# Performance work log

Measured on AMD Instinct MI355X. Metric: run time of the kernel, lower is better.

Reference implementation:

```python
import jax, jax.numpy as jnp
import numpy as np

N_NODES = 50000
N_EDGES = 600000
N_ELEMENTS = 100
N_RBF = 50
D = 128
CUTOFF = 5.0


def setup_inputs() -> dict:
    key = jax.random.key(0)
    ks = jax.random.split(key, 10)
    node_type = jax.random.randint(ks[0], (N_NODES,), 0, N_ELEMENTS)
    x_nodes = jax.random.normal(ks[1], (N_NODES, D), dtype=jnp.float32)
    src = jax.random.randint(ks[2], (N_EDGES,), 0, N_NODES)
    dst = jax.random.randint(ks[3], (N_EDGES,), 0, N_NODES)
    rbf_edges = jax.random.normal(ks[4], (N_EDGES, N_RBF), dtype=jnp.float32)
    dist = jax.random.uniform(ks[5], (N_EDGES,), dtype=jnp.float32) * (CUTOFF * 1.2)
    emb = jax.random.normal(ks[6], (N_ELEMENTS, D), dtype=jnp.float32) * 0.1
    W_e = jax.random.normal(ks[7], (D, N_RBF), dtype=jnp.float32) * (1.0 / np.sqrt(N_RBF))
    b_e = jnp.zeros((D,), dtype=jnp.float32)
    W_c = jax.random.normal(ks[8], (D, 2 * D), dtype=jnp.float32) * (1.0 / np.sqrt(2 * D))
    b_c = jnp.zeros((D,), dtype=jnp.float32)
    return {"node_type": node_type, "x_nodes": x_nodes, "src": src, "dst": dst,
            "rbf_edges": rbf_edges, "dist": dist, "emb": emb,
            "W_e": W_e, "b_e": b_e, "W_c": W_c, "b_c": b_c}


def cosine_cutoff(dist, cutoff):
    # 0.5*(cos(pi*d/cutoff)+1), zeroed beyond cutoff
    w = 0.5 * (jnp.cos(dist * (jnp.pi / cutoff)) + 1.0)
    return w * (dist < cutoff).astype(dist.dtype)


def reference(node_type, x_nodes, src, dst, rbf_edges, dist, emb, W_e, b_e, W_c, b_c):
    # node embedding from atom type: [N, D]
    x_neighbors = emb[node_type]
    # edge projection weighted by cutoff: [E, D]
    x_edges = (rbf_edges @ W_e.T + b_e) * cosine_cutoff(dist, CUTOFF)[:, None]
    # gather source node embedding, multiply by edge embedding, scatter-sum to dst
    msg = x_neighbors[src] * x_edges  # [E, D]
    x_integrated = jax.ops.segment_sum(msg, dst, num_segments=N_NODES)  # [N, D]
    # concat + combine linear: [N, D]
    x_combine = jnp.concatenate([x_nodes, x_integrated], axis=-1)
    return x_combine @ W_c.T + b_c
```

## Files before the change

kernel.cpp:

```cpp
#include <hip/hip_runtime.h>
#include <hip/hip_bf16.h>

constexpr int NN   = 50000;
constexpr int NE   = 600000;
constexpr int NRBF = 50;
constexpr int DIM  = 128;
constexpr float CUT = 5.0f;
constexpr float PI_F = 3.14159265358979323846f;

constexpr int CAP = 32;

constexpr size_t OFF_DEG   = 0;
constexpr size_t OFF_OVFC  = (size_t)NN * 4;
constexpr size_t OFF_EBUF  = 200960;
constexpr size_t OFF_OVF   = OFF_EBUF + (size_t)NN * CAP * 16;
constexpr size_t OFF_WAUG  = OFF_OVF  + (size_t)NE * 4;
constexpr size_t OFF_EPERM = OFF_WAUG + 128 * 64 * 2;
constexpr size_t OFF_WCB   = OFF_EPERM + 100 * 128 * 2;


typedef __attribute__((ext_vector_type(4))) float f32x4;
typedef __attribute__((ext_vector_type(8))) short short8;

__device__ __forceinline__ float bf2f(unsigned short u) {
    return __uint_as_float(((unsigned int)u) << 16);
}
__device__ __forceinline__ unsigned short f2bf(float f) {
    return __bfloat16_as_ushort(__float2bfloat16(f));
}

__global__ __launch_bounds__(256)
void bucket_prep(const int* __restrict__ dst, const float* __restrict__ dist,
                 const int* __restrict__ src, const int* __restrict__ node_type,
                 int* __restrict__ deg, int4* __restrict__ ebuf,
                 int* __restrict__ ovf, int* __restrict__ ovf_cnt,
                 const float* __restrict__ W_e, const float* __restrict__ b_e,
                 const float* __restrict__ emb, const float* __restrict__ W_c,
                 unsigned short* __restrict__ W_aug, unsigned short* __restrict__ emb_perm,
                 unsigned short* __restrict__ W_cb)
{
    const int e = blockIdx.x * 256 + threadIdx.x;

    if (e < NE) {
        const float dd = dist[e];
        if (dd < CUT) {
            const float w = 0.5f * (__cosf(dd * (PI_F / CUT)) + 1.0f);
            const int n = dst[e];
            const int pos = atomicAdd(&deg[n], 1);
            if (pos < CAP) {
                ebuf[(size_t)n * CAP + pos] =
                    make_int4(e, __float_as_int(w), node_type[src[e]], 0);
            } else {
                ovf[atomicAdd(ovf_cnt, 1)] = e;
            }
        }
    }

    if (e < 128 * 64) {
        const int d = e >> 6, k = e & 63;
        float v = 0.0f;
        if (k < NRBF)       v = W_e[d * NRBF + k];
        else if (k == NRBF) v = b_e[d];
        W_aug[e] = f2bf(v);
    } else if (e < 128 * 64 + 100 * 128) {
        const int i = e - 128 * 64;
        const int tau = i >> 7, p = i & 127;
        const int d = 16 * (p & 7) + (p >> 3);
        emb_perm[i] = f2bf(emb[tau * DIM + d]);
    } else if (e < 128 * 64 + 100 * 128 + 128 * 256) {
        const int i = e - (128 * 64 + 100 * 128);
        W_cb[i] = f2bf(W_c[i]);
    }
}

struct NodeLoad {
    float2 r0, r1, r2, r3, q0, q1, q2, q3;
    float  ccl;
    int    degn;
    int    mb;
};

__device__ __forceinline__ void issue_node(const int4* __restrict__ eb_s,
                                           const int* __restrict__ deg_s,
                                           const float* __restrict__ rbf,
                                           int nl, int c, int g, NodeLoad& L)
{
    const int dn = deg_s[nl];
    L.degn = dn < CAP ? dn : CAP;
    L.mb   = nl * 32;
    int ea = 0; L.ccl = 0.0f;
    if (c < L.degn) {
        const int4 eb = eb_s[L.mb + c];
        ea    = eb.x;
        L.ccl = __int_as_float(eb.y);
    }
    const float2* rp2 = (const float2*)(rbf + (size_t)ea * NRBF);
    L.r0 = rp2[4 * g];     L.r1 = rp2[4 * g + 1];
    L.r2 = rp2[4 * g + 2]; L.r3 = rp2[4 * g + 3];
    L.q0 = make_float2(0.f, 0.f); L.q1 = L.q0; L.q2 = L.q0; L.q3 = L.q0;
    if (g < 2) {
        L.q0 = rp2[16 + 4 * g]; L.q1 = rp2[17 + 4 * g];
        L.q2 = rp2[18 + 4 * g]; L.q3 = rp2[19 + 4 * g];
    } else if (g == 2) {
        L.q0 = rp2[24];
    }
}

__device__ __forceinline__ void round_compute(
    float ccl, float2 r0, float2 r1, float2 r2, float2 r3,
    float2 q0, float2 q1, float2 q2, float2 q3,
    int j0, int degn, int mb, int c, int g,
    const unsigned short* __restrict__ wlds, const int4* __restrict__ eb_s,
    const unsigned short* __restrict__ emb_perm, float v[8])
{
    short8 a0, a1;
    a0[0] = (short)f2bf(ccl * r0.x); a0[1] = (short)f2bf(ccl * r0.y);
    a0[2] = (short)f2bf(ccl * r1.x); a0[3] = (short)f2bf(ccl * r1.y);
    a0[4] = (short)f2bf(ccl * r2.x); a0[5] = (short)f2bf(ccl * r2.y);
    a0[6] = (short)f2bf(ccl * r3.x); a0[7] = (short)f2bf(ccl * r3.y);
    a1[0] = (short)f2bf(ccl * q0.x); a1[1] = (short)f2bf(ccl * q0.y);
    a1[2] = (short)f2bf(ccl * q1.x); a1[3] = (short)f2bf(ccl * q1.y);
    a1[4] = (short)f2bf(ccl * q2.x); a1[5] = (short)f2bf(ccl * q2.y);
    a1[6] = (short)f2bf(ccl * q3.x); a1[7] = (short)f2bf(ccl * q3.y);
    if (g == 2) {
        a1[2] = (short)f2bf(ccl);
        a1[3] = 0; a1[4] = 0; a1[5] = 0; a1[6] = 0; a1[7] = 0;
    }

    f32x4 acc[8] = {};
    #pragma unroll
    for (int nt = 0; nt < 8; ++nt) {
        const short8 bf0 = *(const short8*)((const char*)wlds + (nt * 16 + c) * 144 + g * 16);
        acc[nt] = __builtin_amdgcn_mfma_f32_16x16x32_bf16(a0, bf0, acc[nt], 0, 0, 0);
    }
    #pragma unroll
    for (int nt = 0; nt < 8; ++nt) {
        const short8 bf1 = *(const short8*)((const char*)wlds + (nt * 16 + c) * 144 + (4 + g) * 16);
        acc[nt] = __builtin_amdgcn_mfma_f32_16x16x32_bf16(a1, bf1, acc[nt], 0, 0, 0);
    }

    #pragma unroll
    for (int r = 0; r < 4; ++r) {
        const int jr = j0 + 4 * g + r;
        if (jr < degn) {
            const int rw = ((const int*)&eb_s[mb + jr])[2];
            const int4 em = *(const int4*)(emb_perm + rw * DIM + 8 * c);
            const unsigned int* ep = (const unsigned int*)&em;
            #pragma unroll
            for (int q = 0; q < 4; ++q) {
                const float m0 = bf2f((unsigned short)(ep[q] & 0xffff));
                const float m1 = bf2f((unsigned short)(ep[q] >> 16));
                v[2 * q]     += bf2f(f2bf(acc[2 * q][r]     * m0));
                v[2 * q + 1] += bf2f(f2bf(acc[2 * q + 1][r] * m1));
            }
        }
    }
}

__device__ __forceinline__ void compute_node(
    const NodeLoad& L, int c, int g,
    const unsigned short* __restrict__ wlds, const int4* __restrict__ eb_s,
    const unsigned short* __restrict__ emb_perm, const float* __restrict__ rbf,
    float v[8])
{
    round_compute(L.ccl, L.r0, L.r1, L.r2, L.r3, L.q0, L.q1, L.q2, L.q3,
                  0, L.degn, L.mb, c, g, wlds, eb_s, emb_perm, v);
    if (L.degn > 16) {
        int ea = 0; float ccl = 0.0f;
        const int slot = 16 + c;
        if (slot < L.degn) {
            const int4 eb = eb_s[L.mb + slot];
            ea  = eb.x;
            ccl = __int_as_float(eb.y);
        }
        const float2* rp2 = (const float2*)(rbf + (size_t)ea * NRBF);
        const float2 r0 = rp2[4 * g],     r1 = rp2[4 * g + 1];
        const float2 r2 = rp2[4 * g + 2], r3 = rp2[4 * g + 3];
        float2 q0 = make_float2(0.f, 0.f), q1 = q0, q2 = q0, q3 = q0;
        if (g < 2) {
            q0 = rp2[16 + 4 * g]; q1 = rp2[17 + 4 * g];
            q2 = rp2[18 + 4 * g]; q3 = rp2[19 + 4 * g];
        } else if (g == 2) {
            q0 = rp2[24];
        }
        round_compute(ccl, r0, r1, r2, r3, q0, q1, q2, q3,
                      16, L.degn, L.mb, c, g, wlds, eb_s, emb_perm, v);
    }
}

__device__ __forceinline__ void finish_node_lds(
    float v[8], int n, int nl, int c, int g, int ocnt,
    const int* __restrict__ ovf, const int* __restrict__ dst,
    const float* __restrict__ dist, const int* __restrict__ src,
    const int* __restrict__ node_type, const float* __restrict__ rbf,
    const unsigned short* __restrict__ W_aug_g,
    const unsigned short* __restrict__ emb_perm,
    unsigned short* __restrict__ cat_s )
{
    for (int j = 0; j < ocnt; ++j) {
        const int e = ovf[j];
        if (dst[e] != n) continue;
        const float dd  = dist[e];
        const float ccl = 0.5f * (__cosf(dd * (PI_F / CUT)) + 1.0f);
        if (g == 0) {
            const int tau = node_type[src[e]];
            const float* rp = rbf + (size_t)e * NRBF;
            const float ccb16 = bf2f(f2bf(ccl));
            #pragma unroll
            for (int q = 0; q < 8; ++q) {
                const int d = 16 * q + c;
                float s = bf2f(W_aug_g[d * 64 + NRBF]) * ccb16;
                for (int k = 0; k < NRBF; ++k)
                    s += bf2f(W_aug_g[d * 64 + k]) * bf2f(f2bf(ccl * rp[k]));
                v[q] += bf2f(f2bf(s * bf2f(emb_perm[tau * DIM + 8 * c + q])));
            }
        }
    }

    #pragma unroll
    for (int q = 0; q < 8; ++q) {
        v[q] += __shfl_xor(v[q], 16);
        v[q] += __shfl_xor(v[q], 32);
    }

    float s0 = v[0], s1 = v[1];
    if (g == 1)      { s0 = v[2]; s1 = v[3]; }
    else if (g == 2) { s0 = v[4]; s1 = v[5]; }
    else if (g == 3) { s0 = v[6]; s1 = v[7]; }
    cat_s[nl * 264 + 128 + 32 * g + c]      = f2bf(s0);
    cat_s[nl * 264 + 128 + 32 * g + 16 + c] = f2bf(s1);
}

__global__ __launch_bounds__(256)
void gather_combine(const float* __restrict__ rbf,
                    const int* __restrict__ deg, const int4* __restrict__ ebuf,
                    const unsigned short* __restrict__ W_aug,
                    const unsigned short* __restrict__ emb_perm,
                    const unsigned short* __restrict__ W_cb,
                    const int* __restrict__ ovf, const int* __restrict__ ovf_cnt,
                    const int* __restrict__ dst, const float* __restrict__ dist,
                    const int* __restrict__ src, const int* __restrict__ node_type,
                    const float* __restrict__ x_nodes, const float* __restrict__ b_c,
                    float* __restrict__ out)
{
    __shared__ __align__(16) unsigned short wlds[128 * 72];
    __shared__ __align__(16) unsigned short cat_s[16 * 264];
    __shared__ int4 eb_s[8 * 32];
    __shared__ int  deg_s[8];

    const int t = threadIdx.x, l = t & 63;
    const int wv = t >> 6;
    const int c = l & 15, g = l >> 4;
    const int n0 = blockIdx.x * 8;

    {
        eb_s[t] = ebuf[(size_t)n0 * CAP + t];
        if (t < 8) deg_s[t] = deg[n0 + t];
        #pragma unroll
        for (int i = 0; i < 4; ++i) {
            const int ch = i * 256 + t;
            const int row = ch >> 3, f = ch & 7;
            *(int4*)((char*)wlds + row * 144 + f * 16) = ((const int4*)W_aug)[ch];
        }
        const int nl = t >> 5, k0 = (t & 31) * 4;
        const float4 xv = *(const float4*)(x_nodes + (size_t)(n0 + nl) * DIM + k0);
        *(ushort2*)&cat_s[nl * 264 + k0]     = make_ushort2(f2bf(xv.x), f2bf(xv.y));
        *(ushort2*)&cat_s[nl * 264 + k0 + 2] = make_ushort2(f2bf(xv.z), f2bf(xv.w));
    }
    __syncthreads();
    const int ocnt = ovf_cnt[0];

    const int nbase = wv * 2;
    #pragma unroll
    for (int ni = 0; ni < 2; ++ni) {
        const int nl = nbase + ni;
        NodeLoad L;
        issue_node(eb_s, deg_s, rbf, nl, c, g, L);
        float v[8] = {};
        compute_node(L, c, g, wlds, eb_s, emb_perm, rbf, v);
        finish_node_lds(v, n0 + nl, nl, c, g, ocnt, ovf, dst, dist, src,
                        node_type, rbf, W_aug, emb_perm, cat_s);
    }
    __syncthreads();

    f32x4 acc0 = {}, acc1 = {};
    const int t0 = wv * 2, t1 = wv * 2 + 1;
    #pragma unroll
    for (int kc = 0; kc < 8; ++kc) {
        const int ko = kc * 32 + g * 8;
        const short8 af = *(const short8*)&cat_s[c * 264 + ko];
        const short8 b0 = *(const short8*)(W_cb + (size_t)(t0 * 16 + c) * 256 + ko);
        const short8 b1 = *(const short8*)(W_cb + (size_t)(t1 * 16 + c) * 256 + ko);
        acc0 = __builtin_amdgcn_mfma_f32_16x16x32_bf16(af, b0, acc0, 0, 0, 0);
        acc1 = __builtin_amdgcn_mfma_f32_16x16x32_bf16(af, b1, acc1, 0, 0, 0);
    }
    const float bc0 = b_c[t0 * 16 + c];
    const float bc1 = b_c[t1 * 16 + c];
    #pragma unroll
    for (int r = 0; r < 4; ++r) {
        const int node = 4 * g + r;
        if (node < 8) {
            out[(size_t)(n0 + node) * DIM + t0 * 16 + c] = acc0[r] + bc0;
            out[(size_t)(n0 + node) * DIM + t1 * 16 + c] = acc1[r] + bc1;
        }
    }
}

extern "C" void kernel_launch(void* const* d_in, const int* in_sizes, int n_in,
                              void* d_out, int out_size, void* d_ws, size_t ws_size,
                              hipStream_t stream)
{
    const int*   node_type = (const int*)  d_in[0];
    const float* x_nodes   = (const float*)d_in[1];
    const int*   src       = (const int*)  d_in[2];
    const int*   dst       = (const int*)  d_in[3];
    const float* rbf       = (const float*)d_in[4];
    const float* dist      = (const float*)d_in[5];
    const float* emb       = (const float*)d_in[6];
    const float* W_e       = (const float*)d_in[7];
    const float* b_e       = (const float*)d_in[8];
    const float* W_c       = (const float*)d_in[9];
    const float* b_c       = (const float*)d_in[10];
    float* out = (float*)d_out;

    char* ws = (char*)d_ws;
    int*            deg      = (int*)(ws + OFF_DEG);
    int*            ovf_cnt  = (int*)(ws + OFF_OVFC);
    int4*           ebuf     = (int4*)(ws + OFF_EBUF);
    int*            ovf      = (int*)(ws + OFF_OVF);
    unsigned short* W_aug    = (unsigned short*)(ws + OFF_WAUG);
    unsigned short* emb_perm = (unsigned short*)(ws + OFF_EPERM);
    unsigned short* W_cb     = (unsigned short*)(ws + OFF_WCB);

    hipMemsetAsync(deg, 0, (NN + 1) * sizeof(int), stream);

    bucket_prep<<<(NE + 255) / 256, 256, 0, stream>>>(
        dst, dist, src, node_type, deg, ebuf, ovf, ovf_cnt,
        W_e, b_e, emb, W_c, W_aug, emb_perm, W_cb);

    gather_combine<<<NN / 8, 256, 0, stream>>>(
        rbf, deg, ebuf, W_aug, emb_perm, W_cb,
        ovf, ovf_cnt, dst, dist, src, node_type, x_nodes, b_c, out);
}
```

Before: 360.9 us.

## Process 16 nodes per gather block and 4 edges per bucketing thread

The gather_combine kernel now handles 16 nodes per block, with each wave doing 4 nodes. This fills all 16 rows of the MFMA combine tile, which were half empty before, and spreads the per-block W_aug LDS load over twice as many nodes. bucket_prep now has each thread process 4 edges using vectorized int4/float4 loads of dst, dist and src, and it issues the node_type lookups up front. The cost is half as many gather blocks, so less parallelism and latency hiding, and a longer serial chain of node work per wave.

```diff
diff --git a/kernel.cpp b/kernel.cpp
--- a/kernel.cpp
+++ b/kernel.cpp
@@ -39,36 +39,51 @@
                  unsigned short* __restrict__ W_aug, unsigned short* __restrict__ emb_perm,
                  unsigned short* __restrict__ W_cb)
 {
-    const int e = blockIdx.x * 256 + threadIdx.x;
-
-    if (e < NE) {
-        const float dd = dist[e];
-        if (dd < CUT) {
-            const float w = 0.5f * (__cosf(dd * (PI_F / CUT)) + 1.0f);
-            const int n = dst[e];
-            const int pos = atomicAdd(&deg[n], 1);
-            if (pos < CAP) {
-                ebuf[(size_t)n * CAP + pos] =
-                    make_int4(e, __float_as_int(w), node_type[src[e]], 0);
-            } else {
-                ovf[atomicAdd(ovf_cnt, 1)] = e;
+    const int tid = blockIdx.x * 256 + threadIdx.x;
+    const int e0  = tid * 4;
+
+    if (e0 < NE) {
+        const int4   d4 = *(const int4*)(dst + e0);
+        const float4 x4 = *(const float4*)(dist + e0);
+        const int4   s4 = *(const int4*)(src + e0);
+        const int*   dp = (const int*)&d4;
+        const float* xp = (const float*)&x4;
+        const int*   sp = (const int*)&s4;
+
+        int tau[4];
+        #pragma unroll
+        for (int j = 0; j < 4; ++j) tau[j] = node_type[sp[j]];
+
+        #pragma unroll
+        for (int j = 0; j < 4; ++j) {
+            const float dd = xp[j];
+            if (dd < CUT) {
+                const float w = 0.5f * (__cosf(dd * (PI_F / CUT)) + 1.0f);
+                const int n = dp[j];
+                const int pos = atomicAdd(&deg[n], 1);
+                if (pos < CAP) {
+                    ebuf[(size_t)n * CAP + pos] =
+                        make_int4(e0 + j, __float_as_int(w), tau[j], 0);
+                } else {
+                    ovf[atomicAdd(ovf_cnt, 1)] = e0 + j;
+                }
             }
         }
     }
 
-    if (e < 128 * 64) {
-        const int d = e >> 6, k = e & 63;
+    if (tid < 128 * 64) {
+        const int d = tid >> 6, k = tid & 63;
         float v = 0.0f;
         if (k < NRBF)       v = W_e[d * NRBF + k];
         else if (k == NRBF) v = b_e[d];
-        W_aug[e] = f2bf(v);
-    } else if (e < 128 * 64 + 100 * 128) {
-        const int i = e - 128 * 64;
+        W_aug[tid] = f2bf(v);
+    } else if (tid < 128 * 64 + 100 * 128) {
+        const int i = tid - 128 * 64;
         const int tau = i >> 7, p = i & 127;
         const int d = 16 * (p & 7) + (p >> 3);
         emb_perm[i] = f2bf(emb[tau * DIM + d]);
-    } else if (e < 128 * 64 + 100 * 128 + 128 * 256) {
-        const int i = e - (128 * 64 + 100 * 128);
+    } else if (tid < 128 * 64 + 100 * 128 + 128 * 256) {
+        const int i = tid - (128 * 64 + 100 * 128);
         W_cb[i] = f2bf(W_c[i]);
     }
 }
@@ -245,34 +260,39 @@
 {
     __shared__ __align__(16) unsigned short wlds[128 * 72];
     __shared__ __align__(16) unsigned short cat_s[16 * 264];
-    __shared__ int4 eb_s[8 * 32];
-    __shared__ int  deg_s[8];
+    __shared__ int4 eb_s[16 * 32];
+    __shared__ int  deg_s[16];
 
     const int t = threadIdx.x, l = t & 63;
     const int wv = t >> 6;
     const int c = l & 15, g = l >> 4;
-    const int n0 = blockIdx.x * 8;
+    const int n0 = blockIdx.x * 16;
 
     {
-        eb_s[t] = ebuf[(size_t)n0 * CAP + t];
-        if (t < 8) deg_s[t] = deg[n0 + t];
+        eb_s[t]       = ebuf[(size_t)n0 * CAP + t];
+        eb_s[256 + t] = ebuf[(size_t)n0 * CAP + 256 + t];
+        if (t < 16) deg_s[t] = deg[n0 + t];
         #pragma unroll
         for (int i = 0; i < 4; ++i) {
             const int ch = i * 256 + t;
             const int row = ch >> 3, f = ch & 7;
             *(int4*)((char*)wlds + row * 144 + f * 16) = ((const int4*)W_aug)[ch];
         }
-        const int nl = t >> 5, k0 = (t & 31) * 4;
-        const float4 xv = *(const float4*)(x_nodes + (size_t)(n0 + nl) * DIM + k0);
-        *(ushort2*)&cat_s[nl * 264 + k0]     = make_ushort2(f2bf(xv.x), f2bf(xv.y));
-        *(ushort2*)&cat_s[nl * 264 + k0 + 2] = make_ushort2(f2bf(xv.z), f2bf(xv.w));
+        const int nl = t >> 4, k0 = (t & 15) * 8;
+        const float4 xv0 = *(const float4*)(x_nodes + (size_t)(n0 + nl) * DIM + k0);
+        const float4 xv1 = *(const float4*)(x_nodes + (size_t)(n0 + nl) * DIM + k0 + 4);
+        unsigned short* dp = &cat_s[nl * 264 + k0];
+        *(ushort2*)&dp[0] = make_ushort2(f2bf(xv0.x), f2bf(xv0.y));
+        *(ushort2*)&dp[2] = make_ushort2(f2bf(xv0.z), f2bf(xv0.w));
+        *(ushort2*)&dp[4] = make_ushort2(f2bf(xv1.x), f2bf(xv1.y));
+        *(ushort2*)&dp[6] = make_ushort2(f2bf(xv1.z), f2bf(xv1.w));
     }
     __syncthreads();
     const int ocnt = ovf_cnt[0];
 
-    const int nbase = wv * 2;
-    #pragma unroll
-    for (int ni = 0; ni < 2; ++ni) {
+    const int nbase = wv * 4;
+    #pragma unroll
+    for (int ni = 0; ni < 4; ++ni) {
         const int nl = nbase + ni;
         NodeLoad L;
         issue_node(eb_s, deg_s, rbf, nl, c, g, L);
@@ -299,10 +319,8 @@
     #pragma unroll
     for (int r = 0; r < 4; ++r) {
         const int node = 4 * g + r;
-        if (node < 8) {
-            out[(size_t)(n0 + node) * DIM + t0 * 16 + c] = acc0[r] + bc0;
-            out[(size_t)(n0 + node) * DIM + t1 * 16 + c] = acc1[r] + bc1;
-        }
+        out[(size_t)(n0 + node) * DIM + t0 * 16 + c] = acc0[r] + bc0;
+        out[(size_t)(n0 + node) * DIM + t1 * 16 + c] = acc1[r] + bc1;
     }
 }
 
@@ -334,11 +352,11 @@
 
     hipMemsetAsync(deg, 0, (NN + 1) * sizeof(int), stream);
 
-    bucket_prep<<<(NE + 255) / 256, 256, 0, stream>>>(
+    bucket_prep<<<(NE / 4 + 255) / 256, 256, 0, stream>>>(
         dst, dist, src, node_type, deg, ebuf, ovf, ovf_cnt,
         W_e, b_e, emb, W_c, W_aug, emb_perm, W_cb);
 
-    gather_combine<<<NN / 8, 256, 0, stream>>>(
+    gather_combine<<<NN / 16, 256, 0, stream>>>(
         rbf, deg, ebuf, W_aug, emb_perm, W_cb,
         ovf, ovf_cnt, dst, dist, src, node_type, x_nodes, b_c, out);
 }
```

New measurement: 332.8 us. -7.8%, faster.

## Split bucketing into count/place passes, pack edge records to int2, 16 nodes per block

Applied to the files above, without the earlier changes.

Bucketing now runs as two kernels. The first records each edge's atomic slot position, and the second computes the cutoff weight and node type and writes the edge record. Edge records shrink from int4 to int2 by packing the edge index and atom type into one int, which halves ebuf traffic and LDS use. gather_combine now handles 16 nodes per block instead of 8, so the 16-row MFMA in the combine step is fully used and the grid is half as large. In exchange there is an extra kernel launch and an extra pos array write and read. The finish_node_lds overflow path is not shown, so it is unclear whether it was updated for the int2 format.

```diff
diff --git a/kernel.cpp b/kernel.cpp
--- a/kernel.cpp
+++ b/kernel.cpp
@@ -13,7 +13,8 @@
 constexpr size_t OFF_DEG   = 0;
 constexpr size_t OFF_OVFC  = (size_t)NN * 4;
 constexpr size_t OFF_EBUF  = 200960;
-constexpr size_t OFF_OVF   = OFF_EBUF + (size_t)NN * CAP * 16;
+constexpr size_t OFF_POS   = OFF_EBUF + (size_t)NN * CAP * 8;
+constexpr size_t OFF_OVF   = OFF_POS  + (size_t)NE * 4;
 constexpr size_t OFF_WAUG  = OFF_OVF  + (size_t)NE * 4;
 constexpr size_t OFF_EPERM = OFF_WAUG + 128 * 64 * 2;
 constexpr size_t OFF_WCB   = OFF_EPERM + 100 * 128 * 2;
@@ -30,30 +31,19 @@
 }
 
 __global__ __launch_bounds__(256)
-void bucket_prep(const int* __restrict__ dst, const float* __restrict__ dist,
-                 const int* __restrict__ src, const int* __restrict__ node_type,
-                 int* __restrict__ deg, int4* __restrict__ ebuf,
-                 int* __restrict__ ovf, int* __restrict__ ovf_cnt,
-                 const float* __restrict__ W_e, const float* __restrict__ b_e,
-                 const float* __restrict__ emb, const float* __restrict__ W_c,
-                 unsigned short* __restrict__ W_aug, unsigned short* __restrict__ emb_perm,
-                 unsigned short* __restrict__ W_cb)
+void bp_count(const float* __restrict__ dist, const int* __restrict__ dst,
+              int* __restrict__ deg, int* __restrict__ pos,
+              const float* __restrict__ W_e, const float* __restrict__ b_e,
+              const float* __restrict__ emb, const float* __restrict__ W_c,
+              unsigned short* __restrict__ W_aug, unsigned short* __restrict__ emb_perm,
+              unsigned short* __restrict__ W_cb)
 {
     const int e = blockIdx.x * 256 + threadIdx.x;
 
     if (e < NE) {
         const float dd = dist[e];
-        if (dd < CUT) {
-            const float w = 0.5f * (__cosf(dd * (PI_F / CUT)) + 1.0f);
-            const int n = dst[e];
-            const int pos = atomicAdd(&deg[n], 1);
-            if (pos < CAP) {
-                ebuf[(size_t)n * CAP + pos] =
-                    make_int4(e, __float_as_int(w), node_type[src[e]], 0);
-            } else {
-                ovf[atomicAdd(ovf_cnt, 1)] = e;
-            }
-        }
+        if (dd < CUT)
+            pos[e] = atomicAdd(&deg[dst[e]], 1);
     }
 
     if (e < 128 * 64) {
@@ -73,6 +63,26 @@
     }
 }
 
+__global__ __launch_bounds__(256)
+void bp_place(const float* __restrict__ dist, const int* __restrict__ dst,
+              const int* __restrict__ src, const int* __restrict__ node_type,
+              const int* __restrict__ pos, int2* __restrict__ ebuf,
+              int* __restrict__ ovf, int* __restrict__ ovf_cnt)
+{
+    const int e = blockIdx.x * 256 + threadIdx.x;
+    if (e >= NE) return;
+    const float dd = dist[e];
+    if (dd >= CUT) return;
+    const int p = pos[e];
+    if (p < CAP) {
+        const float w = 0.5f * (__cosf(dd * (PI_F / CUT)) + 1.0f);
+        const int tau = node_type[src[e]];
+        ebuf[(size_t)dst[e] * CAP + p] = make_int2((e << 7) | tau, __float_as_int(w));
+    } else {
+        ovf[atomicAdd(ovf_cnt, 1)] = e;
+    }
+}
+
 struct NodeLoad {
     float2 r0, r1, r2, r3, q0, q1, q2, q3;
     float  ccl;
@@ -80,7 +90,7 @@
     int    mb;
 };
 
-__device__ __forceinline__ void issue_node(const int4* __restrict__ eb_s,
+__device__ __forceinline__ void issue_node(const int2* __restrict__ eb_s,
                                            const int* __restrict__ deg_s,
                                            const float* __restrict__ rbf,
                                            int nl, int c, int g, NodeLoad& L)
@@ -90,8 +100,8 @@
     L.mb   = nl * 32;
     int ea = 0; L.ccl = 0.0f;
     if (c < L.degn) {
-        const int4 eb = eb_s[L.mb + c];
-        ea    = eb.x;
+        const int2 eb = eb_s[L.mb + c];
+        ea    = eb.x >> 7;
         L.ccl = __int_as_float(eb.y);
     }
     const float2* rp2 = (const float2*)(rbf + (size_t)ea * NRBF);
@@ -110,7 +120,7 @@
     float ccl, float2 r0, float2 r1, float2 r2, float2 r3,
     float2 q0, float2 q1, float2 q2, float2 q3,
     int j0, int degn, int mb, int c, int g,
-    const unsigned short* __restrict__ wlds, const int4* __restrict__ eb_s,
+    const unsigned short* __restrict__ wlds, const int2* __restrict__ eb_s,
     const unsigned short* __restrict__ emb_perm, float v[8])
 {
     short8 a0, a1;
@@ -143,7 +153,7 @@
     for (int r = 0; r < 4; ++r) {
         const int jr = j0 + 4 * g + r;
         if (jr < degn) {
-            const int rw = ((const int*)&eb_s[mb + jr])[2];
+            const int rw = eb_s[mb + jr].x & 127;
             const int4 em = *(const int4*)(emb_perm + rw * DIM + 8 * c);
             const unsigned int* ep = (const unsigned int*)&em;
             #pragma unroll
@@ -159,7 +169,7 @@
 
 __device__ __forceinline__ void compute_node(
     const NodeLoad& L, int c, int g,
-    const unsigned short* __restrict__ wlds, const int4* __restrict__ eb_s,
+    const unsigned short* __restrict__ wlds, const int2* __restrict__ eb_s,
     const unsigned short* __restrict__ emb_perm, const float* __restrict__ rbf,
     float v[8])
 {
@@ -169,8 +179,8 @@
         int ea = 0; float ccl = 0.0f;
         const int slot = 16 + c;
         if (slot < L.degn) {
-            const int4 eb = eb_s[L.mb + slot];
-            ea  = eb.x;
+            const int2 eb = eb_s[L.mb + slot];
+            ea  = eb.x >> 7;
             ccl = __int_as_float(eb.y);
         }
         const float2* rp2 = (const float2*)(rbf + (size_t)ea * NRBF);
@@ -233,7 +243,7 @@
 
 __global__ __launch_bounds__(256)
 void gather_combine(const float* __restrict__ rbf,
-                    const int* __restrict__ deg, const int4* __restrict__ ebuf,
+                    const int* __restrict__ deg, const int2* __restrict__ ebuf,
                     const unsigned short* __restrict__ W_aug,
                     const unsigned short* __restrict__ emb_perm,
                     const unsigned short* __restrict__ W_cb,
@@ -245,34 +255,39 @@
 {
     __shared__ __align__(16) unsigned short wlds[128 * 72];
     __shared__ __align__(16) unsigned short cat_s[16 * 264];
-    __shared__ int4 eb_s[8 * 32];
-    __shared__ int  deg_s[8];
+    __shared__ int2 eb_s[16 * 32];
+    __shared__ int  deg_s[16];
 
     const int t = threadIdx.x, l = t & 63;
     const int wv = t >> 6;
     const int c = l & 15, g = l >> 4;
-    const int n0 = blockIdx.x * 8;
+    const int n0 = blockIdx.x * 16;
 
     {
-        eb_s[t] = ebuf[(size_t)n0 * CAP + t];
-        if (t < 8) deg_s[t] = deg[n0 + t];
+        eb_s[t]       = ebuf[(size_t)n0 * CAP + t];
+        eb_s[256 + t] = ebuf[(size_t)n0 * CAP + 256 + t];
+        if (t < 16) deg_s[t] = deg[n0 + t];
         #pragma unroll
         for (int i = 0; i < 4; ++i) {
             const int ch = i * 256 + t;
             const int row = ch >> 3, f = ch & 7;
             *(int4*)((char*)wlds + row * 144 + f * 16) = ((const int4*)W_aug)[ch];
         }
-        const int nl = t >> 5, k0 = (t & 31) * 4;
-        const float4 xv = *(const float4*)(x_nodes + (size_t)(n0 + nl) * DIM + k0);
-        *(ushort2*)&cat_s[nl * 264 + k0]     = make_ushort2(f2bf(xv.x), f2bf(xv.y));
-        *(ushort2*)&cat_s[nl * 264 + k0 + 2] = make_ushort2(f2bf(xv.z), f2bf(xv.w));
+        const int nl = t >> 4, k0 = (t & 15) * 8;
+        const float4 xv0 = *(const float4*)(x_nodes + (size_t)(n0 + nl) * DIM + k0);
+        const float4 xv1 = *(const float4*)(x_nodes + (size_t)(n0 + nl) * DIM + k0 + 4);
+        unsigned short* dp = &cat_s[nl * 264 + k0];
+        *(ushort2*)&dp[0] = make_ushort2(f2bf(xv0.x), f2bf(xv0.y));
+        *(ushort2*)&dp[2] = make_ushort2(f2bf(xv0.z), f2bf(xv0.w));
+        *(ushort2*)&dp[4] = make_ushort2(f2bf(xv1.x), f2bf(xv1.y));
+        *(ushort2*)&dp[6] = make_ushort2(f2bf(xv1.z), f2bf(xv1.w));
     }
     __syncthreads();
     const int ocnt = ovf_cnt[0];
 
-    const int nbase = wv * 2;
-    #pragma unroll
-    for (int ni = 0; ni < 2; ++ni) {
+    const int nbase = wv * 4;
+    #pragma unroll
+    for (int ni = 0; ni < 4; ++ni) {
         const int nl = nbase + ni;
         NodeLoad L;
         issue_node(eb_s, deg_s, rbf, nl, c, g, L);
@@ -299,10 +314,8 @@
     #pragma unroll
     for (int r = 0; r < 4; ++r) {
         const int node = 4 * g + r;
-        if (node < 8) {
-            out[(size_t)(n0 + node) * DIM + t0 * 16 + c] = acc0[r] + bc0;
-            out[(size_t)(n0 + node) * DIM + t1 * 16 + c] = acc1[r] + bc1;
-        }
+        out[(size_t)(n0 + node) * DIM + t0 * 16 + c] = acc0[r] + bc0;
+        out[(size_t)(n0 + node) * DIM + t1 * 16 + c] = acc1[r] + bc1;
     }
 }
 
@@ -326,7 +339,8 @@
     char* ws = (char*)d_ws;
     int*            deg      = (int*)(ws + OFF_DEG);
     int*            ovf_cnt  = (int*)(ws + OFF_OVFC);
-    int4*           ebuf     = (int4*)(ws + OFF_EBUF);
+    int2*           ebuf     = (int2*)(ws + OFF_EBUF);
+    int*            pos      = (int*)(ws + OFF_POS);
     int*            ovf      = (int*)(ws + OFF_OVF);
     unsigned short* W_aug    = (unsigned short*)(ws + OFF_WAUG);
     unsigned short* emb_perm = (unsigned short*)(ws + OFF_EPERM);
@@ -334,11 +348,13 @@
 
     hipMemsetAsync(deg, 0, (NN + 1) * sizeof(int), stream);
 
-    bucket_prep<<<(NE + 255) / 256, 256, 0, stream>>>(
-        dst, dist, src, node_type, deg, ebuf, ovf, ovf_cnt,
-        W_e, b_e, emb, W_c, W_aug, emb_perm, W_cb);
-
-    gather_combine<<<NN / 8, 256, 0, stream>>>(
+    bp_count<<<(NE + 255) / 256, 256, 0, stream>>>(
+        dist, dst, deg, pos, W_e, b_e, emb, W_c, W_aug, emb_perm, W_cb);
+
+    bp_place<<<(NE + 255) / 256, 256, 0, stream>>>(
+        dist, dst, src, node_type, pos, ebuf, ovf, ovf_cnt);
+
+    gather_combine<<<NN / 16, 256, 0, stream>>>(
         rbf, deg, ebuf, W_aug, emb_perm, W_cb,
         ovf, ovf_cnt, dst, dist, src, node_type, x_nodes, b_c, out);
 }
```

Result: faster. 333.3 us (-7.7%).
